# Kernel tuning notes

Measured on AMD Instinct MI355X. Metric: run time of the kernel, lower is better.

The kernel has to match this reference:

```python
import jax, jax.numpy as jnp
import numpy as np

HIDDEN = 64
SEQ_LEN = 128
BATCH = 64
T_MAX = 20.0
BW = 1.0


def setup_inputs() -> dict:
    key = jax.random.key(0)
    ks = jax.random.split(key, 8)
    s = 1.0 / np.sqrt(HIDDEN)
    return {
        "rand_uniform_pool": jax.random.uniform(ks[0], (BATCH, SEQ_LEN), jnp.float32, 1e-6, 1.0),
        "expert_time": jax.random.uniform(ks[1], (BATCH, SEQ_LEN), jnp.float32, 0.0, 1.0),
        "W_ih": jax.random.uniform(ks[2], (4 * HIDDEN, 1), jnp.float32, -s, s),
        "W_hh": jax.random.uniform(ks[3], (4 * HIDDEN, HIDDEN), jnp.float32, -s, s),
        "b_ih": jax.random.uniform(ks[4], (4 * HIDDEN,), jnp.float32, -s, s),
        "b_hh": jax.random.uniform(ks[5], (4 * HIDDEN,), jnp.float32, -s, s),
        "V_w": jax.random.uniform(ks[6], (1, HIDDEN), jnp.float32, -s, s),
        "V_b": jax.random.uniform(ks[7], (1,), jnp.float32, -s, s),
    }


def _generate_time(rand_uniform_pool, W_ih, W_hh, b_ih, b_hh, V_w, V_b):
    # sequential rollout over SEQ_LEN steps (data-dependent recurrence)
    u_seq = rand_uniform_pool.T[:, :, None]  # [S, B, 1]

    def step(carry, u):
        hx, cx, cum = carry
        sigma = jax.nn.elu(hx @ V_w.T + V_b) + 1.0            # [B, 1]
        cum = cum + (-jnp.log(u)) / sigma                      # exponential inter-event time
        gates = cum @ W_ih.T + b_ih + hx @ W_hh.T + b_hh       # [B, 4H]
        i, f, g, o = jnp.split(gates, 4, axis=1)               # torch LSTMCell gate order
        cx = jax.nn.sigmoid(f) * cx + jax.nn.sigmoid(i) * jnp.tanh(g)
        hx = jax.nn.sigmoid(o) * jnp.tanh(cx)
        return (hx, cx, cum), cum[:, 0]

    init = (jnp.zeros((BATCH, HIDDEN), jnp.float32),
            jnp.zeros((BATCH, HIDDEN), jnp.float32),
            jnp.zeros((BATCH, 1), jnp.float32))
    _, cums = jax.lax.scan(step, init, u_seq)                  # [S, B]
    return cums.T                                              # [B, S]


def _reward(expert_time, learner_time):
    N = BATCH * SEQ_LEN
    t_l = learner_time.reshape(N)
    t_e = expert_time.reshape(N)
    m_l = ((t_l < T_MAX) & (t_l > 0)).astype(jnp.float32)
    m_e = ((t_e < T_MAX) & (t_e > 0)).astype(jnp.float32)

    def ksum(a, b, ma, mb):
        # ma^T exp(-(a-b)^2/bw) mb without storing more than one NxN matrix at a time
        K = jnp.exp(-((b[:, None] - a[None, :]) ** 2) / BW)    # [N, N]
        return jnp.dot(mb, K @ ma)

    ee = ksum(t_e, t_e, m_e, m_e)
    ll = ksum(t_l, t_l, m_l, m_l)
    le = ksum(t_l, t_e, m_l, m_e)
    return (ee + ll - 2.0 * le).reshape(1, 1)


def reference(rand_uniform_pool, expert_time, W_ih, W_hh, b_ih, b_hh, V_w, V_b):
    learner_time = _generate_time(rand_uniform_pool, W_ih, W_hh, b_ih, b_hh, V_w, V_b)
    loss = _reward(expert_time, learner_time)
    return loss
```

## Files before the change

kernel.cpp:

```cpp
#include <hip/hip_runtime.h>
#include <math.h>

#define HIDDEN 64
#define SEQ 128
#define BATCH 64
#define NPTS (BATCH * SEQ)
#define TMAXV 20.0f
#define L2E 1.4426950408889634f
#define LN2 0.6931471805599453f

typedef float v2f __attribute__((ext_vector_type(2)));

__device__ __forceinline__ float fexp2(float x) { return __builtin_amdgcn_exp2f(x); }
__device__ __forceinline__ float flog2(float x) { return __builtin_amdgcn_logf(x); }
__device__ __forceinline__ float frcp(float x)  { return __builtin_amdgcn_rcpf(x); }
__device__ __forceinline__ float fsigmoid(float x) { return frcp(1.0f + fexp2(-x * L2E)); }
__device__ __forceinline__ float ftanh(float x)    { return 1.0f - 2.0f * frcp(1.0f + fexp2(2.0f * x * L2E)); }

__device__ __forceinline__ void barrier_lds_only() {
    asm volatile("s_waitcnt lgkmcnt(0)" ::: "memory");
    __builtin_amdgcn_s_barrier();
}

template <int CTRL>
__device__ __forceinline__ float dpp_mov(float x) {
    int r = __builtin_amdgcn_update_dpp(0, __float_as_int(x), CTRL, 0xf, 0xf, false);
    return __int_as_float(r);
}
__device__ __forceinline__ float wave_sum_dpp(float x) {
    x += dpp_mov<0x111>(x);
    x += dpp_mov<0x112>(x);
    x += dpp_mov<0x114>(x);
    x += dpp_mov<0x118>(x);
    x += dpp_mov<0x142>(x);
    x += dpp_mov<0x143>(x);
    return __int_as_float(__builtin_amdgcn_readlane(__float_as_int(x), 63));
}

__device__ __forceinline__ float wave_sum_shfl(float v) {
    v += __shfl_xor(v, 1);  v += __shfl_xor(v, 2);  v += __shfl_xor(v, 4);
    v += __shfl_xor(v, 8);  v += __shfl_xor(v, 16); v += __shfl_xor(v, 32);
    return v;
}

__global__ __launch_bounds__(256) void gen_and_ee(
    const float* __restrict__ upool,
    const float* __restrict__ texp,
    const float* __restrict__ Wih,
    const float* __restrict__ Whh,
    const float* __restrict__ bih,
    const float* __restrict__ bhh,
    const float* __restrict__ Vw,
    const float* __restrict__ Vb,
    float* __restrict__ tl,
    float* __restrict__ out)
{
    __shared__ __align__(16) float smem[4288];

    const int bid = blockIdx.x;
    const int tid = threadIdx.x;

    if (bid < BATCH) {
        const int l   = tid & 63;
        const int wv  = tid >> 6;
        const int u   = (wv << 4) + (l >> 2);
        const int g   = l & 3;
        const int row = (g << 6) + u;

        float* hx_s = smem + 4096;
        float* lu_s = smem + 4160;

        v2f w2[32];
        const float4* wrow = (const float4*)(Whh + row * 64);
        #pragma unroll
        for (int k = 0; k < 16; ++k) {
            float4 v = wrow[k];
            w2[2 * k]     = (v2f){v.x, v.y};
            w2[2 * k + 1] = (v2f){v.z, v.w};
        }
        const float bias = bih[row] + bhh[row];
        const float wih  = Wih[row];
        const float vw   = Vw[l];
        const float vb   = Vb[0];

        if (tid < SEQ) lu_s[tid] = -flog2(upool[bid * SEQ + tid]) * LN2;
        if (tid < 64) hx_s[tid] = 0.0f;
        float cx = 0.0f;
        barrier_lds_only();

        float sg0 = (vb > 0.0f) ? (vb + 1.0f) : fexp2(vb * L2E);
        float cum = lu_s[0] * frcp(sg0);
        float keep = (tid == 0) ? cum : 0.0f;

        #pragma unroll 1
        for (int s = 0; s < SEQ - 1; ++s) {
            if (s > 0) {
                float tot = wave_sum_dpp(hx_s[l] * vw);
                float xx  = tot + vb;
                float sg  = (xx > 0.0f) ? (xx + 1.0f) : fexp2(xx * L2E);
                cum += lu_s[s] * frcp(sg);
                keep = (tid == s) ? cum : keep;
            }

            const float4* h4 = (const float4*)hx_s;
            v2f a0 = {0.f, 0.f}, a1 = {0.f, 0.f}, a2 = {0.f, 0.f}, a3 = {0.f, 0.f};
            #pragma unroll
            for (int k = 0; k < 16; k += 2) {
                float4 va = h4[k];
                float4 vbq = h4[k + 1];
                a0 = a0 + w2[2 * k]     * (v2f){va.x, va.y};
                a1 = a1 + w2[2 * k + 1] * (v2f){va.z, va.w};
                a2 = a2 + w2[2 * k + 2] * (v2f){vbq.x, vbq.y};
                a3 = a3 + w2[2 * k + 3] * (v2f){vbq.z, vbq.w};
            }
            v2f aa = (a0 + a1) + (a2 + a3);
            float gin = (aa.x + aa.y) + bias + cum * wih;
            float sig = fsigmoid(gin);
            float tnh = ftanh(gin);
            float a = (g == 2) ? tnh : sig;

            float ig = dpp_mov<0x00>(a);
            float fg = dpp_mov<0x55>(a);
            float gg = dpp_mov<0xAA>(a);
            float og = dpp_mov<0xFF>(a);

            cx = fg * cx + ig * gg;
            float hx = og * ftanh(cx);
            if (g == 0) hx_s[u] = hx;
            barrier_lds_only();
        }
        {
            float tot = wave_sum_dpp(hx_s[l] * vw);
            float xx  = tot + vb;
            float sg  = (xx > 0.0f) ? (xx + 1.0f) : fexp2(xx * L2E);
            cum += lu_s[SEQ - 1] * frcp(sg);
            keep = (tid == SEQ - 1) ? cum : keep;
        }
        if (tid < SEQ) tl[bid * SEQ + tid] = keep;
    } else {
        const int eb = bid - BATCH;
        const int pc = eb & 31;
        const int qs = eb >> 5;

        float2* qbuf = (float2*)smem;

        const int p = pc * 256 + tid;
        const float tp = texp[p];
        const float mp = (tp < TMAXV && tp > 0.0f) ? 1.0f : 0.0f;

        const int q0 = qs * 2048;
        for (int i = tid; i < 2048; i += 256) {
            float tq = texp[q0 + i];
            float mq = (tq < TMAXV && tq > 0.0f) ? 1.0f : 0.0f;
            qbuf[i] = make_float2(tq, mq);
        }
        __syncthreads();

        float acc = 0.0f;
        #pragma unroll 4
        for (int i = 0; i < 2048; ++i) {
            float2 qq = qbuf[i];
            float d = tp - qq.x;
            acc = fmaf(qq.y, fexp2(d * d * (-L2E)), acc);
        }
        acc *= mp;
        acc = wave_sum_shfl(acc);
        if ((tid & 63) == 0) atomicAdd(out, acc);
    }
}

__global__ __launch_bounds__(256) void ll_le(
    const float* __restrict__ texp,
    const float* __restrict__ tl,
    float* __restrict__ out)
{
    __shared__ __align__(16) float4 qbuf[512];
    __shared__ float red[4];

    const int pc = blockIdx.x;
    const int qs = blockIdx.y;
    const int tid = threadIdx.x;

    const int p = pc * 256 + tid;
    const float tlp = tl[p];
    const float mlp = (tlp < TMAXV && tlp > 0.0f) ? 1.0f : 0.0f;

    const int q0 = qs * 512;
    for (int i = tid; i < 512; i += 256) {
        float tq = tl[q0 + i];
        float mq = (tq < TMAXV && tq > 0.0f) ? 1.0f : 0.0f;
        float te = texp[q0 + i];
        float me = (te < TMAXV && te > 0.0f) ? 1.0f : 0.0f;
        qbuf[i] = make_float4(tq, mq, te, me);
    }
    __syncthreads();

    float val = 0.0f;
    if (__ballot(mlp != 0.0f) != 0ULL) {
        float a_ll = 0.0f, a_le = 0.0f;
        #pragma unroll 4
        for (int i = 0; i < 512; ++i) {
            float4 q = qbuf[i];
            float d1 = tlp - q.x;
            a_ll = fmaf(q.y, fexp2(d1 * d1 * (-L2E)), a_ll);
            float d2 = tlp - q.z;
            a_le = fmaf(q.w, fexp2(d2 * d2 * (-L2E)), a_le);
        }
        val = mlp * (a_ll - 2.0f * a_le);
    }

    val = wave_sum_shfl(val);
    if ((tid & 63) == 0) red[tid >> 6] = val;
    __syncthreads();
    if (tid == 0) atomicAdd(out, red[0] + red[1] + red[2] + red[3]);
}

extern "C" void kernel_launch(void* const* d_in, const int* in_sizes, int n_in,
                              void* d_out, int out_size, void* d_ws, size_t ws_size,
                              hipStream_t stream) {
    const float* upool = (const float*)d_in[0];
    const float* texp  = (const float*)d_in[1];
    const float* Wih   = (const float*)d_in[2];
    const float* Whh   = (const float*)d_in[3];
    const float* bih   = (const float*)d_in[4];
    const float* bhh   = (const float*)d_in[5];
    const float* Vw    = (const float*)d_in[6];
    const float* Vb    = (const float*)d_in[7];
    float* out = (float*)d_out;
    float* tl  = (float*)d_ws;

    hipMemsetAsync(out, 0, sizeof(float), stream);
    hipLaunchKernelGGL(gen_and_ee, dim3(BATCH + 128), dim3(256), 0, stream,
                       upool, texp, Wih, Whh, bih, bhh, Vw, Vb, tl, out);
    hipLaunchKernelGGL(ll_le, dim3(32, 16), dim3(256), 0, stream, texp, tl, out);
}
```

Measured before the change: 155.3 us.

## Fuse generation and kernel-sum stages into one cooperative kernel with grid sync

Merges the two launches and the memset into a single cooperative kernel of 192 blocks. The LSTM rollout and ee blocks run first, then a grid-wide sync, then all blocks loop over the 512 ll/le tiles. Zeroing the output moves into the kernel, and ee atomics are deferred until after the sync so they cannot race with that zeroing. This removes launch and memset overhead but runs the ll/le work on fewer blocks and adds the cost of a grid barrier.

```diff
diff --git a/kernel.cpp b/kernel.cpp
--- a/kernel.cpp
+++ b/kernel.cpp
@@ -1,10 +1,14 @@
 #include <hip/hip_runtime.h>
+#include <hip/hip_cooperative_groups.h>
 #include <math.h>
+
+namespace cg = cooperative_groups;
 
 #define HIDDEN 64
 #define SEQ 128
 #define BATCH 64
 #define NPTS (BATCH * SEQ)
+#define NBLK 192
 #define TMAXV 20.0f
 #define L2E 1.4426950408889634f
 #define LN2 0.6931471805599453f
@@ -43,7 +47,7 @@
     return v;
 }
 
-__global__ __launch_bounds__(256) void gen_and_ee(
+__global__ __launch_bounds__(256) void fused(
     const float* __restrict__ upool,
     const float* __restrict__ texp,
     const float* __restrict__ Wih,
@@ -55,10 +59,14 @@
     float* __restrict__ tl,
     float* __restrict__ out)
 {
-    __shared__ __align__(16) float smem[4288];
+    __shared__ __align__(16) float smem[4292];
 
     const int bid = blockIdx.x;
     const int tid = threadIdx.x;
+
+    float ee_partial = 0.0f;
+
+    if (bid == 0 && tid == 0) out[0] = 0.0f;
 
     if (bid < BATCH) {
         const int l   = tid & 63;
@@ -164,55 +172,57 @@
             acc = fmaf(qq.y, fexp2(d * d * (-L2E)), acc);
         }
         acc *= mp;
-        acc = wave_sum_shfl(acc);
-        if ((tid & 63) == 0) atomicAdd(out, acc);
+        ee_partial = wave_sum_shfl(acc);
     }
-}
-
-__global__ __launch_bounds__(256) void ll_le(
-    const float* __restrict__ texp,
-    const float* __restrict__ tl,
-    float* __restrict__ out)
-{
-    __shared__ __align__(16) float4 qbuf[512];
-    __shared__ float red[4];
-
-    const int pc = blockIdx.x;
-    const int qs = blockIdx.y;
-    const int tid = threadIdx.x;
-
-    const int p = pc * 256 + tid;
-    const float tlp = tl[p];
-    const float mlp = (tlp < TMAXV && tlp > 0.0f) ? 1.0f : 0.0f;
-
-    const int q0 = qs * 512;
-    for (int i = tid; i < 512; i += 256) {
-        float tq = tl[q0 + i];
-        float mq = (tq < TMAXV && tq > 0.0f) ? 1.0f : 0.0f;
-        float te = texp[q0 + i];
-        float me = (te < TMAXV && te > 0.0f) ? 1.0f : 0.0f;
-        qbuf[i] = make_float4(tq, mq, te, me);
+
+    cg::this_grid().sync();
+
+    if (bid >= BATCH && (tid & 63) == 0) atomicAdd(out, ee_partial);
+
+    {
+        float4* qbuf4 = (float4*)smem;
+        float*  red   = smem + 4288;
+
+        for (int t = bid; t < 512; t += NBLK) {
+            const int pc = t & 31;
+            const int qs = t >> 5;
+
+            __syncthreads();
+
+            const int p = pc * 256 + tid;
+            const float tlp = tl[p];
+            const float mlp = (tlp < TMAXV && tlp > 0.0f) ? 1.0f : 0.0f;
+
+            const int q0 = qs * 512;
+            for (int i = tid; i < 512; i += 256) {
+                float tq = tl[q0 + i];
+                float mq = (tq < TMAXV && tq > 0.0f) ? 1.0f : 0.0f;
+                float te = texp[q0 + i];
+                float me = (te < TMAXV && te > 0.0f) ? 1.0f : 0.0f;
+                qbuf4[i] = make_float4(tq, mq, te, me);
+            }
+            __syncthreads();
+
+            float val = 0.0f;
+            if (__ballot(mlp != 0.0f) != 0ULL) {
+                float a_ll = 0.0f, a_le = 0.0f;
+                #pragma unroll 4
+                for (int i = 0; i < 512; ++i) {
+                    float4 q = qbuf4[i];
+                    float d1 = tlp - q.x;
+                    a_ll = fmaf(q.y, fexp2(d1 * d1 * (-L2E)), a_ll);
+                    float d2 = tlp - q.z;
+                    a_le = fmaf(q.w, fexp2(d2 * d2 * (-L2E)), a_le);
+                }
+                val = mlp * (a_ll - 2.0f * a_le);
+            }
+
+            val = wave_sum_shfl(val);
+            if ((tid & 63) == 0) red[tid >> 6] = val;
+            __syncthreads();
+            if (tid == 0) atomicAdd(out, red[0] + red[1] + red[2] + red[3]);
+        }
     }
-    __syncthreads();
-
-    float val = 0.0f;
-    if (__ballot(mlp != 0.0f) != 0ULL) {
-        float a_ll = 0.0f, a_le = 0.0f;
-        #pragma unroll 4
-        for (int i = 0; i < 512; ++i) {
-            float4 q = qbuf[i];
-            float d1 = tlp - q.x;
-            a_ll = fmaf(q.y, fexp2(d1 * d1 * (-L2E)), a_ll);
-            float d2 = tlp - q.z;
-            a_le = fmaf(q.w, fexp2(d2 * d2 * (-L2E)), a_le);
-        }
-        val = mlp * (a_ll - 2.0f * a_le);
-    }
-
-    val = wave_sum_shfl(val);
-    if ((tid & 63) == 0) red[tid >> 6] = val;
-    __syncthreads();
-    if (tid == 0) atomicAdd(out, red[0] + red[1] + red[2] + red[3]);
 }
 
 extern "C" void kernel_launch(void* const* d_in, const int* in_sizes, int n_in,
@@ -229,8 +239,8 @@
     float* out = (float*)d_out;
     float* tl  = (float*)d_ws;
 
-    hipMemsetAsync(out, 0, sizeof(float), stream);
-    hipLaunchKernelGGL(gen_and_ee, dim3(BATCH + 128), dim3(256), 0, stream,
-                       upool, texp, Wih, Whh, bih, bhh, Vw, Vb, tl, out);
-    hipLaunchKernelGGL(ll_le, dim3(32, 16), dim3(256), 0, stream, texp, tl, out);
-}
+    void* args[] = {(void*)&upool, (void*)&texp, (void*)&Wih, (void*)&Whh,
+                    (void*)&bih, (void*)&bhh, (void*)&Vw, (void*)&Vb,
+                    (void*)&tl, (void*)&out};
+    hipLaunchCooperativeKernel((void*)fused, dim3(NBLK), dim3(256), args, 0, stream);
+}
```

Measured after the change: 225.5 us. +45.2%, slower.
